# Kernel optimization log

Measured on AMD Instinct MI355X. Metric: run time of the kernel, lower is better.

Reference implementation:

```python
import jax, jax.numpy as jnp
import numpy as np

MAX_WAVELENGTH = 10000.0
NUM_HEADS = 15
NUM_KV_HEADS = 5
HEAD_DIM = 64


def apply_rope(x, positions):
    """RoPE: x [B, L, H, D], positions [B, L] (int)."""
    d_half = x.shape[-1] // 2
    x = x.astype(jnp.float32)
    freq_exponents = (2.0 / x.shape[-1]) * jnp.arange(d_half, dtype=jnp.float32)
    timescale = MAX_WAVELENGTH ** freq_exponents  # [d_half]
    radians = positions[..., None].astype(jnp.float32) / timescale  # [B, L, d_half]
    radians = radians[..., None, :]  # [B, L, 1, d_half]
    sin, cos = jnp.sin(radians), jnp.cos(radians)
    x1, x2 = x[..., :d_half], x[..., d_half:]
    return jnp.concatenate([x1 * cos - x2 * sin, x2 * cos + x1 * sin], axis=-1)


def setup_inputs() -> dict:
    key = jax.random.key(0)
    k1, k2, k3, k4 = jax.random.split(key, 4)
    B, L = 2, 2048
    query_states = jax.random.normal(k1, (B, L, NUM_HEADS, HEAD_DIM), dtype=jnp.float32)
    key_states = jax.random.normal(k2, (B, L, NUM_KV_HEADS, HEAD_DIM), dtype=jnp.float32)
    value_states = jax.random.normal(k3, (B, L, NUM_KV_HEADS, HEAD_DIM), dtype=jnp.float32)
    positions = jnp.sort(jax.random.randint(k4, (B, L), 0, L, dtype=jnp.int32), axis=-1)
    # Causal (prefix-LM) boolean mask [B, L, L]
    attention_mask = jnp.broadcast_to(jnp.tril(jnp.ones((L, L), dtype=bool)), (B, L, L))
    return {
        "query_states": query_states,
        "key_states": key_states,
        "value_states": value_states,
        "positions": positions,
        "attention_mask": attention_mask,
    }


def reference(query_states, key_states, value_states, positions, attention_mask):
    B, L = query_states.shape[0], query_states.shape[1]
    groups = NUM_HEADS // NUM_KV_HEADS  # 3

    # RoPE on Q and K (eager, per original module)
    q = apply_rope(query_states, positions)  # [B, L, 15, 64] fp32
    k = apply_rope(key_states, positions)    # [B, L, 5, 64]  fp32

    # GQA expansion: [B, L, Kv, D] -> [B, L, Kv*groups, D]
    k = jnp.repeat(k, groups, axis=2)
    v = jnp.repeat(value_states, groups, axis=2).astype(jnp.float32)

    # Scores in fp32: [B, H, Lq, Lk]
    scores = jnp.einsum("bqhd,bkhd->bhqk", q, k) * (HEAD_DIM ** -0.5)
    big_neg = jnp.finfo(jnp.float32).min
    scores = jnp.where(attention_mask[:, None, :, :], scores, big_neg)
    probs = jax.nn.softmax(scores, axis=-1)

    out = jnp.einsum("bhqk,bkhd->bqhd", probs, v)  # [B, L, H, D]
    return out.reshape(B, L, NUM_HEADS * HEAD_DIM)  # [B, L, 960]
```

## Files before the change

kernel.cpp:

```cpp
#include <hip/hip_runtime.h>
#include <math.h>

#define NB 2
#define NL 2048
#define NHQ 15
#define NKV 5
#define HD 64
#define NT 32
#define GRP 3
#define PST 72
#define NWB 40
#define CST 68
#define CSLOT (32 * CST + 32)

typedef __attribute__((ext_vector_type(8))) short short8;
typedef __attribute__((ext_vector_type(4))) float floatx4;

#define ROPE_C 0.28782313662425575f
#define QSCALE 0.18033688011116016f

__device__ __forceinline__ ushort f2bf(float x) {
    unsigned u = __builtin_bit_cast(unsigned, x);
    u = (u + 0x7FFFu + ((u >> 16) & 1u)) >> 16;
    return (ushort)u;
}
__device__ __forceinline__ unsigned cvtpk(float a, float b) {
    unsigned r;
    asm("v_cvt_pk_bf16_f32 %0, %1, %2" : "=v"(r) : "v"(a), "v"(b));
    return r;
}

union U8  { short8 v; ushort u[8]; };
union F8  { float4 f4[2]; float f[8]; };

__global__ __launch_bounds__(256)
void prep_kv(const float* __restrict__ K, const float* __restrict__ V,
             const int* __restrict__ pos, ushort* __restrict__ Kr,
             ushort* __restrict__ Vr, float* __restrict__ Tc,
             float* __restrict__ Ts) {
    __shared__ float Vs[64][65];
    const int bid = blockIdx.x, t = threadIdx.x;
    if (bid < NB * NKV * NT) {
        int b = bid / (NKV * NT), rem = bid % (NKV * NT);
        int h = rem / NT, k0 = (rem % NT) * 64;
        int j = t >> 2, c0 = t & 3;
        int row = k0 + j;
        const float* src = K + ((size_t)((b * NL + row) * NKV + h)) * HD;
        int db = c0 * 8;
        F8 x1, x2;
        x1.f4[0] = *(const float4*)&src[db];
        x1.f4[1] = *(const float4*)&src[db + 4];
        x2.f4[0] = *(const float4*)&src[db + 32];
        x2.f4[1] = *(const float4*)&src[db + 36];
        float ps = (float)pos[b * NL + row];
        U8 lo, hi; F8 snv, csv;
#pragma unroll
        for (int i = 0; i < 8; ++i) {
            float inv = __expf((float)(db + i) * -ROPE_C);
            float sn, cs; __sincosf(ps * inv, &sn, &cs);
            snv.f[i] = sn; csv.f[i] = cs;
            lo.u[i] = f2bf(x1.f[i] * cs - x2.f[i] * sn);
            hi.u[i] = f2bf(x2.f[i] * cs + x1.f[i] * sn);
        }
        ushort* dst = Kr + (size_t)bid * 4096;
        *(short8*)&dst[(((j >> 4)) * 64 + c0 * 16 + (j & 15)) * 8]     = lo.v;
        *(short8*)&dst[((4 + (j >> 4)) * 64 + c0 * 16 + (j & 15)) * 8] = hi.v;
        if (rem < NT) {
            float* tcp = Tc + ((size_t)(b * NL + row)) * 32 + db;
            float* tsp = Ts + ((size_t)(b * NL + row)) * 32 + db;
            *(float4*)&tcp[0] = csv.f4[0];
            *(float4*)&tcp[4] = csv.f4[1];
            *(float4*)&tsp[0] = snv.f4[0];
            *(float4*)&tsp[4] = snv.f4[1];
        }
    } else {
        int vb = bid - NB * NKV * NT;
        int b = vb / (NKV * NT), rem = vb % (NKV * NT);
        int h = rem / NT, k0 = (rem % NT) * 64;
#pragma unroll
        for (int it = 0; it < 4; ++it) {
            int e = t + it * 256;
            int j = e >> 4, d4 = (e & 15) * 4;
            *(float4*)&Vs[j][d4] =
                *(const float4*)&V[((size_t)((b * NL + k0 + j) * NKV + h)) * HD + d4];
        }
        __syncthreads();
        ushort* dst = Vr + (size_t)vb * 4096;
#pragma unroll
        for (int it = 0; it < 2; ++it) {
            int o = t + it * 256;
            int d = o >> 3, c = o & 7, j0 = c * 8;
            U8 r;
#pragma unroll
            for (int k = 0; k < 8; ++k) r.u[k] = f2bf(Vs[j0 + k][d]);
            *(short8*)&dst[(((c >> 2) * 4 + (d >> 4)) * 64 + (c & 3) * 16 + (d & 15)) * 8] = r.v;
        }
    }
}

template<bool DIAG>
__device__ __forceinline__ void tile_step(
    int kb, int r0, int l16, int quad, int lane,
    const ushort* Kt0, const ushort* Vt0,
    const short8 (&Qa)[2][2], floatx4 (&O)[2][4], float (&lsum)[2],
    ushort* PbW)
{
    const ushort* kt = Kt0 + (size_t)kb * 4096;
    const ushort* vt = Vt0 + (size_t)kb * 4096;
    short8 kc[8], vc[8];
#pragma unroll
    for (int i = 0; i < 8; ++i)
        kc[i] = *(const short8*)&kt[((size_t)i * 64 + lane) * 8];
#pragma unroll
    for (int i = 0; i < 8; ++i)
        vc[i] = *(const short8*)&vt[((size_t)i * 64 + lane) * 8];

    floatx4 S[2][4];
#pragma unroll
    for (int rf = 0; rf < 2; ++rf)
#pragma unroll
        for (int c = 0; c < 4; ++c) S[rf][c] = (floatx4){0.f, 0.f, 0.f, 0.f};
#pragma unroll
    for (int s = 0; s < 2; ++s)
#pragma unroll
        for (int c = 0; c < 4; ++c) {
            short8 kfv = kc[s * 4 + c];
            S[0][c] = __builtin_amdgcn_mfma_f32_16x16x32_bf16(kfv, Qa[0][s], S[0][c], 0, 0, 0);
            S[1][c] = __builtin_amdgcn_mfma_f32_16x16x32_bf16(kfv, Qa[1][s], S[1][c], 0, 0, 0);
        }

#pragma unroll
    for (int rf = 0; rf < 2; ++rf) {
        int qrow = r0 + rf * 16 + l16;
        float acc = 0.f;
#pragma unroll
        for (int c = 0; c < 4; ++c) {
            float pv[4];
#pragma unroll
            for (int r = 0; r < 4; ++r) {
                float sv = S[rf][c][r];
                if (DIAG) {
                    int key = kb * 64 + c * 16 + quad * 4 + r;
                    if (key > qrow) sv = -1e30f;
                }
                pv[r] = exp2f(sv);
                acc += pv[r];
            }
            *(uint2*)&PbW[rf * 16 * PST + l16 * PST + c * 16 + quad * 4] =
                make_uint2(cvtpk(pv[0], pv[1]), cvtpk(pv[2], pv[3]));
        }
        lsum[rf] += acc;
    }

#pragma unroll
    for (int s = 0; s < 2; ++s) {
        short8 pf0 = *(const short8*)&PbW[0 * 16 * PST + l16 * PST + s * 32 + quad * 8];
        short8 pf1 = *(const short8*)&PbW[1 * 16 * PST + l16 * PST + s * 32 + quad * 8];
#pragma unroll
        for (int d = 0; d < 4; ++d) {
            short8 vfv = vc[s * 4 + d];
            O[0][d] = __builtin_amdgcn_mfma_f32_16x16x32_bf16(vfv, pf0, O[0][d], 0, 0, 0);
            O[1][d] = __builtin_amdgcn_mfma_f32_16x16x32_bf16(vfv, pf1, O[1][d], 0, 0, 0);
        }
    }
}

__global__ __launch_bounds__(256, 3)
void attn_flash(const float* __restrict__ Q, const ushort* __restrict__ Kr,
                const ushort* __restrict__ Vr, const float* __restrict__ Tc,
                const float* __restrict__ Ts, float* __restrict__ out) {
    __shared__ __align__(16) unsigned char smem[3 * CSLOT * sizeof(float)];

    const int t = threadIdx.x;
    const int w = t >> 6, lane = t & 63;
    const int l16 = lane & 15, quad = lane >> 4;

    const int bid  = blockIdx.x;
    const int work = (bid & 7) * 150 + (bid >> 3);
    const int bh   = work / NWB;
    const int beta = work % NWB;
    const int b = bh / NHQ, h = bh % NHQ;
    const int kvh = h / GRP;

    int qi, leaderw, nch;
    if (beta < 16)      { qi = 48 + beta; leaderw = 0; nch = 4; }
    else if (beta < 32) {
        if (w < 3)      { qi = 32 + (beta - 16); leaderw = 0; nch = 3; }
        else            { qi = beta - 16;        leaderw = 3; nch = 1; }
    } else {
        int c = beta - 32;
        if (w < 2)      { qi = 16 + 2 * c; leaderw = 0; nch = 2; }
        else            { qi = 17 + 2 * c; leaderw = 2; nch = 2; }
    }
    const int ntw   = (qi >> 1) + 1;
    const int chunk = w - leaderw;
    const int kb0   = (ntw * chunk) / nch;
    const int kb1   = (ntw * (chunk + 1)) / nch;
    const int r0    = qi * 32;

    const ushort* Kt0 = Kr + (size_t)((b * NKV + kvh) * NT) * 4096;
    const ushort* Vt0 = Vr + (size_t)((b * NKV + kvh) * NT) * 4096;
    ushort* PbW = (ushort*)smem + w * 2 * 16 * PST;

    short8 Qa[2][2];
#pragma unroll
    for (int rf = 0; rf < 2; ++rf) {
        int row = r0 + rf * 16 + l16;
        const float* src = Q + ((size_t)((b * NL + row) * NHQ + h)) * HD;
        int db = quad * 8;
        F8 x1, x2, cs8, sn8;
        x1.f4[0] = *(const float4*)&src[db];
        x1.f4[1] = *(const float4*)&src[db + 4];
        x2.f4[0] = *(const float4*)&src[db + 32];
        x2.f4[1] = *(const float4*)&src[db + 36];
        const float* tcp = Tc + ((size_t)(b * NL + row)) * 32 + db;
        const float* tsp = Ts + ((size_t)(b * NL + row)) * 32 + db;
        cs8.f4[0] = *(const float4*)&tcp[0];
        cs8.f4[1] = *(const float4*)&tcp[4];
        sn8.f4[0] = *(const float4*)&tsp[0];
        sn8.f4[1] = *(const float4*)&tsp[4];
        union { short8 v; unsigned u[4]; } lo, hi;
#pragma unroll
        for (int i = 0; i < 8; i += 2) {
            float lo0 = (x1.f[i] * cs8.f[i] - x2.f[i] * sn8.f[i]) * QSCALE;
            float lo1 = (x1.f[i + 1] * cs8.f[i + 1] - x2.f[i + 1] * sn8.f[i + 1]) * QSCALE;
            float hi0 = (x2.f[i] * cs8.f[i] + x1.f[i] * sn8.f[i]) * QSCALE;
            float hi1 = (x2.f[i + 1] * cs8.f[i + 1] + x1.f[i + 1] * sn8.f[i + 1]) * QSCALE;
            lo.u[i >> 1] = cvtpk(lo0, lo1);
            hi.u[i >> 1] = cvtpk(hi0, hi1);
        }
        Qa[rf][0] = lo.v;
        Qa[rf][1] = hi.v;
    }

    floatx4 O[2][4];
    float lsum[2] = {0.f, 0.f};
#pragma unroll
    for (int rf = 0; rf < 2; ++rf)
#pragma unroll
        for (int d = 0; d < 4; ++d) O[rf][d] = (floatx4){0.f, 0.f, 0.f, 0.f};

    const int kbe = (kb1 == ntw) ? ntw - 1 : kb1;
    for (int kb = kb0; kb < kbe; ++kb)
        tile_step<false>(kb, r0, l16, quad, lane, Kt0, Vt0, Qa, O, lsum, PbW);
    if (kb1 == ntw)
        tile_step<true>(ntw - 1, r0, l16, quad, lane, Kt0, Vt0, Qa, O, lsum, PbW);

    float ls[2];
#pragma unroll
    for (int rf = 0; rf < 2; ++rf) {
        float v = lsum[rf];
        v += __shfl_xor(v, 16, 64);
        v += __shfl_xor(v, 32, 64);
        ls[rf] = v;
    }

    __syncthreads();
    float* Cmb = (float*)smem;
    if (chunk > 0) {
        float* slot = Cmb + (size_t)(w - 1) * CSLOT;
#pragma unroll
        for (int rf = 0; rf < 2; ++rf) {
#pragma unroll
            for (int d = 0; d < 4; ++d) {
                *(float4*)&slot[(rf * 16 + l16) * CST + d * 16 + quad * 4] =
                    make_float4(O[rf][d][0], O[rf][d][1], O[rf][d][2], O[rf][d][3]);
            }
            if (quad == 0) slot[32 * CST + rf * 16 + l16] = ls[rf];
        }
    }
    __syncthreads();
    if (chunk == 0) {
        for (int m = 1; m < nch; ++m) {
            const float* slot = Cmb + (size_t)(w + m - 1) * CSLOT;
#pragma unroll
            for (int rf = 0; rf < 2; ++rf) {
#pragma unroll
                for (int d = 0; d < 4; ++d) {
                    float4 x = *(const float4*)&slot[(rf * 16 + l16) * CST + d * 16 + quad * 4];
                    O[rf][d][0] += x.x; O[rf][d][1] += x.y;
                    O[rf][d][2] += x.z; O[rf][d][3] += x.w;
                }
                ls[rf] += slot[32 * CST + rf * 16 + l16];
            }
        }
#pragma unroll
        for (int rf = 0; rf < 2; ++rf) {
            float rinv = 1.0f / ls[rf];
            int qrow = r0 + rf * 16 + l16;
            float* op = out + (size_t)(b * NL + qrow) * (NHQ * HD) + h * HD;
#pragma unroll
            for (int d = 0; d < 4; ++d) {
                float4 o = make_float4(O[rf][d][0] * rinv, O[rf][d][1] * rinv,
                                       O[rf][d][2] * rinv, O[rf][d][3] * rinv);
                *(float4*)&op[d * 16 + quad * 4] = o;
            }
        }
    }
}

extern "C" void kernel_launch(void* const* d_in, const int* in_sizes, int n_in,
                              void* d_out, int out_size, void* d_ws, size_t ws_size,
                              hipStream_t stream) {
    const float* Q   = (const float*)d_in[0];
    const float* K   = (const float*)d_in[1];
    const float* V   = (const float*)d_in[2];
    const int*   pos = (const int*)d_in[3];
    ushort* Kr = (ushort*)d_ws;
    ushort* Vr = Kr + (size_t)NB * NKV * NT * 4096;
    float*  Tc = (float*)(Vr + (size_t)NB * NKV * NT * 4096);
    float*  Ts = Tc + (size_t)NB * NL * 32;
    float*  out = (float*)d_out;

    prep_kv<<<2 * NB * NKV * NT, 256, 0, stream>>>(K, V, pos, Kr, Vr, Tc, Ts);
    attn_flash<<<NB * NHQ * NWB, 256, 0, stream>>>(Q, Kr, Vr, Tc, Ts, out);
}
```

Before: 141.0 us.

## Process 64 query rows per wave to reuse K/V tiles across two row groups

Each wave now owns a 64-row query block (four 16-row fragments) instead of 32 rows, so every K and V tile fetched from global memory feeds twice as many MFMAs. The tile step interleaves the score MFMAs for the second half with the softmax of the first half, and loads V after the first QK product. The work mapping is halved to 20 units per (batch, head) with the same split-K chunking, and the cross-wave combine runs in two passes to fit the existing shared-memory slots. In exchange, register pressure grows, occupancy is lowered from 3 to 2 blocks per CU, and there are fewer, coarser blocks, which may hurt load balance.

```diff
diff --git a/kernel.cpp b/kernel.cpp
--- a/kernel.cpp
+++ b/kernel.cpp
@@ -9,7 +9,7 @@
 #define NT 32
 #define GRP 3
 #define PST 72
-#define NWB 40
+#define NWB 20
 #define CST 68
 #define CSLOT (32 * CST + 32)
 
@@ -102,18 +102,15 @@
 __device__ __forceinline__ void tile_step(
     int kb, int r0, int l16, int quad, int lane,
     const ushort* Kt0, const ushort* Vt0,
-    const short8 (&Qa)[2][2], floatx4 (&O)[2][4], float (&lsum)[2],
+    const short8 (&Qa)[4][2], floatx4 (&O)[4][4], float (&lsum)[4],
     ushort* PbW)
 {
     const ushort* kt = Kt0 + (size_t)kb * 4096;
     const ushort* vt = Vt0 + (size_t)kb * 4096;
-    short8 kc[8], vc[8];
+    short8 kc[8];
 #pragma unroll
     for (int i = 0; i < 8; ++i)
         kc[i] = *(const short8*)&kt[((size_t)i * 64 + lane) * 8];
-#pragma unroll
-    for (int i = 0; i < 8; ++i)
-        vc[i] = *(const short8*)&vt[((size_t)i * 64 + lane) * 8];
 
     floatx4 S[2][4];
 #pragma unroll
@@ -128,6 +125,11 @@
             S[0][c] = __builtin_amdgcn_mfma_f32_16x16x32_bf16(kfv, Qa[0][s], S[0][c], 0, 0, 0);
             S[1][c] = __builtin_amdgcn_mfma_f32_16x16x32_bf16(kfv, Qa[1][s], S[1][c], 0, 0, 0);
         }
+
+    short8 vc[8];
+#pragma unroll
+    for (int i = 0; i < 8; ++i)
+        vc[i] = *(const short8*)&vt[((size_t)i * 64 + lane) * 8];
 
 #pragma unroll
     for (int rf = 0; rf < 2; ++rf) {
@@ -152,6 +154,20 @@
         lsum[rf] += acc;
     }
 
+    floatx4 T[2][4];
+#pragma unroll
+    for (int rf = 0; rf < 2; ++rf)
+#pragma unroll
+        for (int c = 0; c < 4; ++c) T[rf][c] = (floatx4){0.f, 0.f, 0.f, 0.f};
+#pragma unroll
+    for (int s = 0; s < 2; ++s)
+#pragma unroll
+        for (int c = 0; c < 4; ++c) {
+            short8 kfv = kc[s * 4 + c];
+            T[0][c] = __builtin_amdgcn_mfma_f32_16x16x32_bf16(kfv, Qa[2][s], T[0][c], 0, 0, 0);
+            T[1][c] = __builtin_amdgcn_mfma_f32_16x16x32_bf16(kfv, Qa[3][s], T[1][c], 0, 0, 0);
+        }
+
 #pragma unroll
     for (int s = 0; s < 2; ++s) {
         short8 pf0 = *(const short8*)&PbW[0 * 16 * PST + l16 * PST + s * 32 + quad * 8];
@@ -163,9 +179,44 @@
             O[1][d] = __builtin_amdgcn_mfma_f32_16x16x32_bf16(vfv, pf1, O[1][d], 0, 0, 0);
         }
     }
-}
-
-__global__ __launch_bounds__(256, 3)
+
+#pragma unroll
+    for (int rf = 0; rf < 2; ++rf) {
+        int qrow = r0 + 32 + rf * 16 + l16;
+        float acc = 0.f;
+#pragma unroll
+        for (int c = 0; c < 4; ++c) {
+            float pv[4];
+#pragma unroll
+            for (int r = 0; r < 4; ++r) {
+                float sv = T[rf][c][r];
+                if (DIAG) {
+                    int key = kb * 64 + c * 16 + quad * 4 + r;
+                    if (key > qrow) sv = -1e30f;
+                }
+                pv[r] = exp2f(sv);
+                acc += pv[r];
+            }
+            *(uint2*)&PbW[rf * 16 * PST + l16 * PST + c * 16 + quad * 4] =
+                make_uint2(cvtpk(pv[0], pv[1]), cvtpk(pv[2], pv[3]));
+        }
+        lsum[2 + rf] += acc;
+    }
+
+#pragma unroll
+    for (int s = 0; s < 2; ++s) {
+        short8 pf0 = *(const short8*)&PbW[0 * 16 * PST + l16 * PST + s * 32 + quad * 8];
+        short8 pf1 = *(const short8*)&PbW[1 * 16 * PST + l16 * PST + s * 32 + quad * 8];
+#pragma unroll
+        for (int d = 0; d < 4; ++d) {
+            short8 vfv = vc[s * 4 + d];
+            O[2][d] = __builtin_amdgcn_mfma_f32_16x16x32_bf16(vfv, pf0, O[2][d], 0, 0, 0);
+            O[3][d] = __builtin_amdgcn_mfma_f32_16x16x32_bf16(vfv, pf1, O[3][d], 0, 0, 0);
+        }
+    }
+}
+
+__global__ __launch_bounds__(256, 2)
 void attn_flash(const float* __restrict__ Q, const ushort* __restrict__ Kr,
                 const ushort* __restrict__ Vr, const float* __restrict__ Tc,
                 const float* __restrict__ Ts, float* __restrict__ out) {
@@ -176,36 +227,35 @@
     const int l16 = lane & 15, quad = lane >> 4;
 
     const int bid  = blockIdx.x;
-    const int work = (bid & 7) * 150 + (bid >> 3);
+    const int work = (bid & 7) * 75 + (bid >> 3);
     const int bh   = work / NWB;
     const int beta = work % NWB;
     const int b = bh / NHQ, h = bh % NHQ;
     const int kvh = h / GRP;
 
-    int qi, leaderw, nch;
-    if (beta < 16)      { qi = 48 + beta; leaderw = 0; nch = 4; }
-    else if (beta < 32) {
-        if (w < 3)      { qi = 32 + (beta - 16); leaderw = 0; nch = 3; }
-        else            { qi = beta - 16;        leaderw = 3; nch = 1; }
+    int sj, chunk, nch;
+    if (beta < 8)       { sj = 24 + beta; chunk = w; nch = 4; }
+    else if (beta < 16) {
+        if (w < 3)      { sj = 16 + (beta - 8); chunk = w; nch = 3; }
+        else            { sj = beta - 8;        chunk = 0; nch = 1; }
     } else {
-        int c = beta - 32;
-        if (w < 2)      { qi = 16 + 2 * c; leaderw = 0; nch = 2; }
-        else            { qi = 17 + 2 * c; leaderw = 2; nch = 2; }
-    }
-    const int ntw   = (qi >> 1) + 1;
-    const int chunk = w - leaderw;
-    const int kb0   = (ntw * chunk) / nch;
-    const int kb1   = (ntw * (chunk + 1)) / nch;
-    const int r0    = qi * 32;
+        int c = beta - 16;
+        if (w < 2)      { sj = 8 + 2 * c; chunk = w;     nch = 2; }
+        else            { sj = 9 + 2 * c; chunk = w - 2; nch = 2; }
+    }
+    const int ntw = sj + 1;
+    const int kb0 = (ntw * chunk) / nch;
+    const int kb1 = (ntw * (chunk + 1)) / nch;
+    const int r0  = sj * 64;
 
     const ushort* Kt0 = Kr + (size_t)((b * NKV + kvh) * NT) * 4096;
     const ushort* Vt0 = Vr + (size_t)((b * NKV + kvh) * NT) * 4096;
     ushort* PbW = (ushort*)smem + w * 2 * 16 * PST;
 
-    short8 Qa[2][2];
-#pragma unroll
-    for (int rf = 0; rf < 2; ++rf) {
-        int row = r0 + rf * 16 + l16;
+    short8 Qa[4][2];
+#pragma unroll
+    for (int f = 0; f < 4; ++f) {
+        int row = r0 + f * 16 + l16;
         const float* src = Q + ((size_t)((b * NL + row) * NHQ + h)) * HD;
         int db = quad * 8;
         F8 x1, x2, cs8, sn8;
@@ -229,16 +279,16 @@
             lo.u[i >> 1] = cvtpk(lo0, lo1);
             hi.u[i >> 1] = cvtpk(hi0, hi1);
         }
-        Qa[rf][0] = lo.v;
-        Qa[rf][1] = hi.v;
-    }
-
-    floatx4 O[2][4];
-    float lsum[2] = {0.f, 0.f};
-#pragma unroll
-    for (int rf = 0; rf < 2; ++rf)
-#pragma unroll
-        for (int d = 0; d < 4; ++d) O[rf][d] = (floatx4){0.f, 0.f, 0.f, 0.f};
+        Qa[f][0] = lo.v;
+        Qa[f][1] = hi.v;
+    }
+
+    floatx4 O[4][4];
+    float lsum[4] = {0.f, 0.f, 0.f, 0.f};
+#pragma unroll
+    for (int f = 0; f < 4; ++f)
+#pragma unroll
+        for (int d = 0; d < 4; ++d) O[f][d] = (floatx4){0.f, 0.f, 0.f, 0.f};
 
     const int kbe = (kb1 == ntw) ? ntw - 1 : kb1;
     for (int kb = kb0; kb < kbe; ++kb)
@@ -246,54 +296,60 @@
     if (kb1 == ntw)
         tile_step<true>(ntw - 1, r0, l16, quad, lane, Kt0, Vt0, Qa, O, lsum, PbW);
 
-    float ls[2];
-#pragma unroll
-    for (int rf = 0; rf < 2; ++rf) {
-        float v = lsum[rf];
+    float ls[4];
+#pragma unroll
+    for (int f = 0; f < 4; ++f) {
+        float v = lsum[f];
         v += __shfl_xor(v, 16, 64);
         v += __shfl_xor(v, 32, 64);
-        ls[rf] = v;
-    }
-
-    __syncthreads();
+        ls[f] = v;
+    }
+
     float* Cmb = (float*)smem;
-    if (chunk > 0) {
-        float* slot = Cmb + (size_t)(w - 1) * CSLOT;
-#pragma unroll
-        for (int rf = 0; rf < 2; ++rf) {
-#pragma unroll
-            for (int d = 0; d < 4; ++d) {
-                *(float4*)&slot[(rf * 16 + l16) * CST + d * 16 + quad * 4] =
-                    make_float4(O[rf][d][0], O[rf][d][1], O[rf][d][2], O[rf][d][3]);
+#pragma unroll
+    for (int hf = 0; hf < 2; ++hf) {
+        __syncthreads();
+        if (chunk > 0) {
+            float* slot = Cmb + (size_t)(w - 1) * CSLOT;
+#pragma unroll
+            for (int rf = 0; rf < 2; ++rf) {
+                int f = hf * 2 + rf;
+#pragma unroll
+                for (int d = 0; d < 4; ++d) {
+                    *(float4*)&slot[(rf * 16 + l16) * CST + d * 16 + quad * 4] =
+                        make_float4(O[f][d][0], O[f][d][1], O[f][d][2], O[f][d][3]);
+                }
+                if (quad == 0) slot[32 * CST + rf * 16 + l16] = ls[f];
             }
-            if (quad == 0) slot[32 * CST + rf * 16 + l16] = ls[rf];
-        }
-    }
-    __syncthreads();
-    if (chunk == 0) {
-        for (int m = 1; m < nch; ++m) {
-            const float* slot = Cmb + (size_t)(w + m - 1) * CSLOT;
+        }
+        __syncthreads();
+        if (chunk == 0) {
 #pragma unroll
             for (int rf = 0; rf < 2; ++rf) {
+                int f = hf * 2 + rf;
+                floatx4 acc[4];
+#pragma unroll
+                for (int d = 0; d < 4; ++d) acc[d] = O[f][d];
+                float lsv = ls[f];
+                for (int m = 1; m < nch; ++m) {
+                    const float* slot = Cmb + (size_t)(w + m - 1) * CSLOT;
+#pragma unroll
+                    for (int d = 0; d < 4; ++d) {
+                        float4 x = *(const float4*)&slot[(rf * 16 + l16) * CST + d * 16 + quad * 4];
+                        acc[d][0] += x.x; acc[d][1] += x.y;
+                        acc[d][2] += x.z; acc[d][3] += x.w;
+                    }
+                    lsv += slot[32 * CST + rf * 16 + l16];
+                }
+                float rinv = 1.0f / lsv;
+                int qrow = r0 + hf * 32 + rf * 16 + l16;
+                float* op = out + (size_t)(b * NL + qrow) * (NHQ * HD) + h * HD;
 #pragma unroll
                 for (int d = 0; d < 4; ++d) {
-                    float4 x = *(const float4*)&slot[(rf * 16 + l16) * CST + d * 16 + quad * 4];
-                    O[rf][d][0] += x.x; O[rf][d][1] += x.y;
-                    O[rf][d][2] += x.z; O[rf][d][3] += x.w;
-                }
-                ls[rf] += slot[32 * CST + rf * 16 + l16];
-            }
-        }
-#pragma unroll
-        for (int rf = 0; rf < 2; ++rf) {
-            float rinv = 1.0f / ls[rf];
-            int qrow = r0 + rf * 16 + l16;
-            float* op = out + (size_t)(b * NL + qrow) * (NHQ * HD) + h * HD;
-#pragma unroll
-            for (int d = 0; d < 4; ++d) {
-                float4 o = make_float4(O[rf][d][0] * rinv, O[rf][d][1] * rinv,
-                                       O[rf][d][2] * rinv, O[rf][d][3] * rinv);
-                *(float4*)&op[d * 16 + quad * 4] = o;
+                    float4 o = make_float4(acc[d][0] * rinv, acc[d][1] * rinv,
+                                           acc[d][2] * rinv, acc[d][3] * rinv);
+                    *(float4*)&op[d * 16 + quad * 4] = o;
+                }
             }
         }
     }
```

Measured after the change: 146.3 us. +3.7%, slower.
